# Kernel optimization log

Hardware: AMD Instinct MI355X
Metric: run time of the kernel (lower is better)

Reference implementation:

```python
import jax, jax.numpy as jnp
import numpy as np
from jax import lax

# Quantization params from symmetric_linear_quantization_params(num_bits=5, sat=9):
# n = 2**(5-1)-1 = 15, scale = 15/9, zero_point = 0
Q_SCALE = 15.0 / 9.0
Q_ZP = 0.0


def ste_quant_dequant(y, scale=Q_SCALE, zp=Q_ZP):
    # forward: round(scale*y - zp); dequant: (q + zp)/scale. backward: identity (STE).
    q = jnp.round(scale * y - zp)
    dq = (q + zp) / scale
    return y + lax.stop_gradient(dq - y)


def setup_inputs() -> dict:
    key = jax.random.key(0)
    k1, k2, k3 = jax.random.split(key, 3)
    B, Cin, H, Wd = 8, 16, 112, 112
    Cout, KH, KW = 32, 3, 3
    x = jax.random.normal(k1, (B, Cin, H, Wd), dtype=jnp.float32)
    # per-input-channel conv weights: [Cin, Cout, 1, KH, KW]
    W = jax.random.normal(k2, (Cin, Cout, 1, KH, KW), dtype=jnp.float32) * (1.0 / np.sqrt(KH * KW))
    b = jax.random.normal(k3, (Cin, Cout), dtype=jnp.float32) * 0.1
    return {"x": x, "W": W, "b": b}


def reference(x, W, b):
    B, Cin, H, Wd = x.shape
    Cout = W.shape[1]
    # Fuse the in_channels separate 1->Cout convs into one grouped conv:
    # weight [Cin*Cout, 1, KH, KW], feature_group_count=Cin
    w_grouped = W.reshape(Cin * Cout, 1, W.shape[3], W.shape[4])
    y = lax.conv_general_dilated(
        x, w_grouped,
        window_strides=(1, 1),
        padding=((1, 1), (1, 1)),
        dimension_numbers=("NCHW", "OIHW", "NCHW"),
        feature_group_count=Cin,
    )  # [B, Cin*Cout, H, W]
    y = y.reshape(B, Cin, Cout, y.shape[2], y.shape[3])
    y = y + b[None, :, :, None, None]
    # quantize-dequant each per-input-channel partial output, then sum over Cin
    out = jnp.sum(ste_quant_dequant(y), axis=1)  # [B, Cout, H, W]
    return out
```

## Files before the change

kernel.cpp:

```cpp
#include <hip/hip_runtime.h>


constexpr int B_    = 8;
constexpr int CIN   = 16;
constexpr int COUT  = 32;
constexpr int H_    = 112;
constexpr int W_    = 112;
constexpr int TILE  = 16;
constexpr int HALO  = TILE + 2;
constexpr int LDSW  = HALO + 2;
constexpr int COG   = 8;

__global__ __launch_bounds__(256, 6)
void conv_quant_sum_kernel(const float* __restrict__ x,
                           const float* __restrict__ w,
                           const float* __restrict__ bias,
                           float* __restrict__ out)
{
#pragma clang fp contract(off)
    const float QS  = (float)(15.0 / 9.0);
    const float DQI = 0.6f;

    __shared__ float xs[CIN][HALO][LDSW];

    const int tx = threadIdx.x & 15;
    const int ty = threadIdx.x >> 4;
    const int tile_x = blockIdx.x * TILE;
    const int tile_y = blockIdx.y * TILE;
    const int b   = blockIdx.z >> 2;
    const int cog = (blockIdx.z & 3) * COG;

    const float* xb = x + (size_t)b * CIN * H_ * W_;
    for (int idx = threadIdx.x; idx < CIN * HALO * HALO; idx += 256) {
        int ci  = idx / (HALO * HALO);
        int rem = idx - ci * (HALO * HALO);
        int r   = rem / HALO;
        int c   = rem - r * HALO;
        int gh  = tile_y + r - 1;
        int gw  = tile_x + c - 1;
        float v = 0.0f;
        if ((unsigned)gh < (unsigned)H_ && (unsigned)gw < (unsigned)W_)
            v = xb[ci * H_ * W_ + gh * W_ + gw];
        xs[ci][r][c] = v;
    }
    __syncthreads();

    float acc[COG];
#pragma unroll
    for (int co = 0; co < COG; ++co) acc[co] = 0.0f;

    for (int ci = 0; ci < CIN; ++ci) {
        float xv[9];
#pragma unroll
        for (int kh = 0; kh < 3; ++kh)
#pragma unroll
            for (int kw = 0; kw < 3; ++kw)
                xv[kh * 3 + kw] = xs[ci][ty + kh][tx + kw];

        const float* wc = w + (ci * COUT + cog) * 9;
        const float* bc = bias + ci * COUT + cog;
#pragma unroll
        for (int co = 0; co < COG; ++co) {
            float s = 0.0f;
#pragma unroll
            for (int k = 0; k < 9; ++k)
                s = fmaf(xv[k], wc[co * 9 + k], s);
            float y = s + bc[co];
            float q = rintf(y * QS);
            acc[co] = fmaf(q, DQI, acc[co]);
        }
    }

    float* ob = out + ((size_t)b * COUT + cog) * H_ * W_;
    const int oh = tile_y + ty;
    const int ow = tile_x + tx;
#pragma unroll
    for (int co = 0; co < COG; ++co)
        ob[co * H_ * W_ + oh * W_ + ow] = acc[co];
}

extern "C" void kernel_launch(void* const* d_in, const int* in_sizes, int n_in,
                              void* d_out, int out_size, void* d_ws, size_t ws_size,
                              hipStream_t stream)
{
    const float* x    = (const float*)d_in[0];
    const float* w    = (const float*)d_in[1];
    const float* bias = (const float*)d_in[2];
    float* out        = (float*)d_out;

    dim3 grid(W_ / TILE, H_ / TILE, B_ * 4);
    dim3 block(256);
    conv_quant_sum_kernel<<<grid, block, 0, stream>>>(x, w, bias, out);
}
```

Measured before the change: 97.64 us.

## Compute two adjacent pixels per thread with packed FMA and split channel groups

Each thread now computes two horizontally adjacent output pixels for four output channels, using 2-wide float vectors so the compiler can emit packed FMA instructions. The two halves of the block cover different channel subgroups, and the input window is reused across neighbouring pixels, which cuts LDS reads per output. Output stores become 8-byte vector writes. The LDS row pitch changes to 21, which may alter bank-conflict behaviour, and rounding stays scalar per lane.

```diff
diff --git a/kernel.cpp b/kernel.cpp
--- a/kernel.cpp
+++ b/kernel.cpp
@@ -1,5 +1,7 @@
 #include <hip/hip_runtime.h>
 
+
+typedef float v2f __attribute__((ext_vector_type(2)));
 
 constexpr int B_    = 8;
 constexpr int CIN   = 16;
@@ -8,8 +10,8 @@
 constexpr int W_    = 112;
 constexpr int TILE  = 16;
 constexpr int HALO  = TILE + 2;
-constexpr int LDSW  = HALO + 2;
-constexpr int COG   = 8;
+constexpr int LDSW  = 21;
+constexpr int COG   = 4;
 
 __global__ __launch_bounds__(256, 6)
 void conv_quant_sum_kernel(const float* __restrict__ x,
@@ -18,20 +20,22 @@
                            float* __restrict__ out)
 {
 #pragma clang fp contract(off)
-    const float QS  = (float)(15.0 / 9.0);
-    const float DQI = 0.6f;
+    const float QS = (float)(15.0 / 9.0);
+    const float DQ = 0.6f;
 
     __shared__ float xs[CIN][HALO][LDSW];
 
-    const int tx = threadIdx.x & 15;
-    const int ty = threadIdx.x >> 4;
+    const int t    = threadIdx.x;
+    const int tx   = t & 7;
+    const int ty   = (t >> 3) & 15;
+    const int half = t >> 7;
     const int tile_x = blockIdx.x * TILE;
     const int tile_y = blockIdx.y * TILE;
-    const int b   = blockIdx.z >> 2;
-    const int cog = (blockIdx.z & 3) * COG;
+    const int b    = blockIdx.z >> 2;
+    const int cog  = (blockIdx.z & 3) * 8 + half * COG;
 
     const float* xb = x + (size_t)b * CIN * H_ * W_;
-    for (int idx = threadIdx.x; idx < CIN * HALO * HALO; idx += 256) {
+    for (int idx = t; idx < CIN * HALO * HALO; idx += 256) {
         int ci  = idx / (HALO * HALO);
         int rem = idx - ci * (HALO * HALO);
         int r   = rem / HALO;
@@ -45,38 +49,52 @@
     }
     __syncthreads();
 
-    float acc[COG];
+    v2f acc[COG];
 #pragma unroll
-    for (int co = 0; co < COG; ++co) acc[co] = 0.0f;
+    for (int co = 0; co < COG; ++co) acc[co] = v2f{0.0f, 0.0f};
 
     for (int ci = 0; ci < CIN; ++ci) {
-        float xv[9];
+        float xr[3][4];
 #pragma unroll
-        for (int kh = 0; kh < 3; ++kh)
+        for (int r = 0; r < 3; ++r)
 #pragma unroll
-            for (int kw = 0; kw < 3; ++kw)
-                xv[kh * 3 + kw] = xs[ci][ty + kh][tx + kw];
+            for (int c = 0; c < 4; ++c)
+                xr[r][c] = xs[ci][ty + r][2 * tx + c];
+
+        v2f xw[3][3];
+#pragma unroll
+        for (int r = 0; r < 3; ++r) {
+            xw[r][0] = v2f{xr[r][0], xr[r][1]};
+            xw[r][1] = v2f{xr[r][1], xr[r][2]};
+            xw[r][2] = v2f{xr[r][2], xr[r][3]};
+        }
 
         const float* wc = w + (ci * COUT + cog) * 9;
         const float* bc = bias + ci * COUT + cog;
 #pragma unroll
         for (int co = 0; co < COG; ++co) {
-            float s = 0.0f;
+            v2f s = v2f{0.0f, 0.0f};
 #pragma unroll
-            for (int k = 0; k < 9; ++k)
-                s = fmaf(xv[k], wc[co * 9 + k], s);
-            float y = s + bc[co];
-            float q = rintf(y * QS);
-            acc[co] = fmaf(q, DQI, acc[co]);
+            for (int k = 0; k < 9; ++k) {
+                float wv = wc[co * 9 + k];
+                s = __builtin_elementwise_fma(xw[k / 3][k % 3], v2f{wv, wv}, s);
+            }
+            float bv = bc[co];
+            v2f y  = s + v2f{bv, bv};
+            v2f tq = y * v2f{QS, QS};
+            v2f q;
+            q.x = rintf(tq.x);
+            q.y = rintf(tq.y);
+            acc[co] = __builtin_elementwise_fma(q, v2f{DQ, DQ}, acc[co]);
         }
     }
 
     float* ob = out + ((size_t)b * COUT + cog) * H_ * W_;
     const int oh = tile_y + ty;
-    const int ow = tile_x + tx;
+    const int ow = tile_x + 2 * tx;
 #pragma unroll
     for (int co = 0; co < COG; ++co)
-        ob[co * H_ * W_ + oh * W_ + ow] = acc[co];
+        *reinterpret_cast<v2f*>(ob + co * H_ * W_ + oh * W_ + ow) = acc[co];
 }
 
 extern "C" void kernel_launch(void* const* d_in, const int* in_sizes, int n_in,
```

Measured after the change: 107.6 us. 10.2% more time.
